# Performance work log

Hardware: AMD Instinct MI355X
Metric: run time of the kernel (lower is better)

The kernel has to match this reference:

```python
import jax, jax.numpy as jnp
import numpy as np

N_NODES = 10000
N_EDGES = 160000
D = 512            # input_dim = hidden_size = output_dim
NUM_EXPERTS = 4
N_LAYERS = 2


def setup_inputs() -> dict:
    key = jax.random.key(0)
    k = jax.random.split(key, 7)
    x = jax.random.normal(k[0], (N_NODES, D), dtype=jnp.float32)
    edge_index = jax.random.randint(k[1], (2, N_EDGES), 0, N_NODES, dtype=jnp.int32)
    # Gating network (Linear D -> NUM_EXPERTS)
    gate_w = jax.random.normal(k[2], (D, NUM_EXPERTS), dtype=jnp.float32) * 0.05
    gate_b = jnp.zeros((NUM_EXPERTS,), dtype=jnp.float32)
    # Per-expert SAGEConv weights: lin_r (self/root) and lin_l (neighbor) + bias
    w_self = jax.random.normal(k[3], (NUM_EXPERTS, N_LAYERS, D, D), dtype=jnp.float32) * 0.05
    w_neigh = jax.random.normal(k[4], (NUM_EXPERTS, N_LAYERS, D, D), dtype=jnp.float32) * 0.05
    b_exp = jnp.zeros((NUM_EXPERTS, N_LAYERS, D), dtype=jnp.float32)
    return {"x": x, "edge_index": edge_index, "gate_w": gate_w, "gate_b": gate_b,
            "w_self": w_self, "w_neigh": w_neigh, "b_exp": b_exp, "top_k": 1}


def reference(x, edge_index, gate_w, gate_b, w_self, w_neigh, b_exp, top_k):
    n = x.shape[0]
    src, dst = edge_index[0], edge_index[1]
    # mean-aggregation normalization (PyG SAGEConv aggr='mean'); 0 for isolated nodes
    deg = jax.ops.segment_sum(jnp.ones_like(src, dtype=x.dtype), dst, num_segments=n)
    inv_deg = jnp.where(deg > 0, 1.0 / jnp.maximum(deg, 1.0), 0.0)[:, None]  # [N,1]

    # gating: softmax(Linear(x)) then top-k routing
    gate = jax.nn.softmax(x @ gate_w + gate_b, axis=-1)          # [N, E]
    top_vals, top_idx = jax.lax.top_k(gate, top_k)               # [N, k]

    def expert(ws, wn, b):  # ws, wn: [L, D, D]; b: [L, D]
        h = x
        for l in range(N_LAYERS):
            agg = jax.ops.segment_sum(h[src], dst, num_segments=n) * inv_deg
            # SAGEConv: lin_l(mean_neigh) + lin_r(x) + bias, then relu (norm='id', eval dropout)
            h = jax.nn.relu(agg @ wn[l] + h @ ws[l] + b[l])
        return h

    # dense all-expert compute (matches original module)
    outs = jax.vmap(expert)(w_self, w_neigh, b_exp)              # [E, N, D]
    outs = jnp.transpose(outs, (1, 0, 2))                        # [N, E, D]
    sel = jnp.take_along_axis(outs, top_idx[:, :, None], axis=1)  # [N, k, D]
    return jnp.sum(sel * top_vals[:, :, None], axis=1)           # [N, D]
```

## Files before the change

kernel.cpp:

```cpp
#include <hip/hip_runtime.h>
#include <hip/hip_bf16.h>
#include <cstdint>

#define N_NODES 10000
#define N_EDGES 160000
#define DIM 512
#define K1 1024
#define NEXP 4

typedef __bf16 bf16_t;
typedef bf16_t bf16x8 __attribute__((ext_vector_type(8)));
typedef float f32x4 __attribute__((ext_vector_type(4)));

#define AS1(p) ((__attribute__((address_space(1))) void*)(p))
#define AS3(p) ((__attribute__((address_space(3))) void*)(p))

#define VMW(N) asm volatile("s_waitcnt vmcnt(" #N ")" ::: "memory")

__global__ void zero_kernel(int* __restrict__ deg, int* __restrict__ ecnt) {
    int i = blockIdx.x * blockDim.x + threadIdx.x;
    if (i < N_NODES) deg[i] = 0;
    if (i < NEXP) ecnt[i] = 0;
}

__global__ void gate_kernel(const float* __restrict__ x,
                            const float* __restrict__ gw,
                            const float* __restrict__ gb,
                            int* __restrict__ top_idx,
                            float* __restrict__ top_val,
                            bf16_t* __restrict__ acat) {
    const int wave = threadIdx.x >> 6;
    const int lane = threadIdx.x & 63;
    const int node = blockIdx.x * 4 + wave;
    if (node >= N_NODES) return;
    const float4* x4 = (const float4*)(x + (size_t)node * DIM);
    const float4* gw4 = (const float4*)gw;
    float4 xa = x4[lane * 2];
    float4 xb = x4[lane * 2 + 1];
    float xv[8] = { xa.x, xa.y, xa.z, xa.w, xb.x, xb.y, xb.z, xb.w };
    float a0 = 0.f, a1 = 0.f, a2 = 0.f, a3 = 0.f;
    #pragma unroll
    for (int c = 0; c < 8; c++) {
        float4 g = gw4[lane * 8 + c];
        a0 += xv[c] * g.x; a1 += xv[c] * g.y; a2 += xv[c] * g.z; a3 += xv[c] * g.w;
    }
    bf16x8 o;
    #pragma unroll
    for (int c = 0; c < 8; c++) o[c] = (bf16_t)xv[c];
    *(bf16x8*)(acat + (size_t)node * K1 + DIM + lane * 8) = o;
    for (int off = 32; off > 0; off >>= 1) {
        a0 += __shfl_xor(a0, off);
        a1 += __shfl_xor(a1, off);
        a2 += __shfl_xor(a2, off);
        a3 += __shfl_xor(a3, off);
    }
    if (lane == 0) {
        float z[4] = { a0 + gb[0], a1 + gb[1], a2 + gb[2], a3 + gb[3] };
        int bi = 0; float bm = z[0];
        for (int e = 1; e < 4; e++) if (z[e] > bm) { bm = z[e]; bi = e; }
        float den = 0.f;
        for (int e = 0; e < 4; e++) den += expf(z[e] - bm);
        top_idx[node] = bi;
        top_val[node] = 1.0f / den;
    }
}

__global__ void bucket_kernel(const int* __restrict__ top_idx,
                              int* __restrict__ ecnt,
                              int* __restrict__ lists) {
    __shared__ int lcnt[NEXP];
    __shared__ int base[NEXP];
    const int tid = threadIdx.x;
    if (tid < NEXP) lcnt[tid] = 0;
    __syncthreads();
    const int node = blockIdx.x * 256 + tid;
    int e = 0, rank = 0;
    if (node < N_NODES) {
        e = top_idx[node];
        rank = atomicAdd(&lcnt[e], 1);
    }
    __syncthreads();
    if (tid < NEXP) base[tid] = atomicAdd(&ecnt[tid], lcnt[tid]);
    __syncthreads();
    if (node < N_NODES) lists[e * N_NODES + base[e] + rank] = node;
}

__global__ void deg_kernel(const int* __restrict__ dst, int* __restrict__ deg) {
    int i = blockIdx.x * blockDim.x + threadIdx.x;
    if (i < N_EDGES) atomicAdd(&deg[dst[i]], 1);
}

__global__ void scan_kernel(const int* __restrict__ deg,
                            int* __restrict__ offs,
                            int* __restrict__ cursor) {
    __shared__ int wsum[16];
    __shared__ int carrysh;
    const int tid = threadIdx.x;
    const int lane = tid & 63;
    const int wv = tid >> 6;
    if (tid == 0) carrysh = 0;
    __syncthreads();
    for (int base = 0; base < N_NODES; base += 1024) {
        int i = base + tid;
        int v = (i < N_NODES) ? deg[i] : 0;
        int s = v;
        #pragma unroll
        for (int off = 1; off < 64; off <<= 1) {
            int t = __shfl_up(s, off);
            if (lane >= off) s += t;
        }
        if (lane == 63) wsum[wv] = s;
        int carry = carrysh;
        __syncthreads();
        if (wv == 0) {
            int w = (lane < 16) ? wsum[lane] : 0;
            #pragma unroll
            for (int off = 1; off < 16; off <<= 1) {
                int t = __shfl_up(w, off);
                if (lane >= off) w += t;
            }
            if (lane < 16) wsum[lane] = w;
        }
        __syncthreads();
        int wbase = (wv > 0) ? wsum[wv - 1] : 0;
        int excl = carry + wbase + s - v;
        if (i < N_NODES) { offs[i] = excl; cursor[i] = excl; }
        int total = wsum[15];
        __syncthreads();
        if (tid == 0) carrysh = carry + total;
        __syncthreads();
    }
    if (tid == 0) offs[N_NODES] = carrysh;
}

__global__ void fill_kernel(const int* __restrict__ src, const int* __restrict__ dst,
                            int* __restrict__ cursor, int* __restrict__ csr) {
    int i = blockIdx.x * blockDim.x + threadIdx.x;
    if (i < N_EDGES) {
        int d = dst[i];
        int p = atomicAdd(&cursor[d], 1);
        csr[p] = src[i];
    }
}

__global__ void wtrans_kernel(const float* __restrict__ w_neigh,
                              const float* __restrict__ w_self,
                              bf16_t* __restrict__ Bt) {
    __shared__ float tile[32][33];
    const int m = blockIdx.z;
    const bool isSelf = m >= 8;
    const int el = m & 7;
    const float* W = (isSelf ? w_self : w_neigh) + (size_t)el * DIM * DIM;
    const int k0 = blockIdx.x * 32;
    const int n0 = blockIdx.y * 32;
    const int tx = threadIdx.x, ty = threadIdx.y;
    for (int r = ty; r < 32; r += 8)
        tile[r][tx] = W[(size_t)(k0 + r) * DIM + n0 + tx];
    __syncthreads();
    for (int r = ty; r < 32; r += 8) {
        int n = n0 + r;
        int k = k0 + tx;
        Bt[((size_t)el * DIM + n) * K1 + (isSelf ? DIM : 0) + k] = (bf16_t)tile[tx][r];
    }
}

__global__ void agg1_kernel(const int* __restrict__ offs, const int* __restrict__ csr,
                            bf16_t* __restrict__ acat) {
    const int wave = threadIdx.x >> 6;
    const int lane = threadIdx.x & 63;
    const int node = blockIdx.x * 4 + wave;
    if (node >= N_NODES) return;
    const int c0 = lane * 8;
    float s[8] = {0,0,0,0,0,0,0,0};
    int beg = offs[node];
    int end = offs[node + 1];
    int d = end - beg;
    int p = beg;
    for (; p + 8 <= end; p += 8) {
        bf16x8 v[8];
        #pragma unroll
        for (int q = 0; q < 8; q++) {
            int idx = csr[p + q];
            v[q] = *(const bf16x8*)(acat + (size_t)idx * K1 + DIM + c0);
        }
        #pragma unroll
        for (int q = 0; q < 8; q++)
            #pragma unroll
            for (int k = 0; k < 8; k++) s[k] += (float)v[q][k];
    }
    for (; p + 4 <= end; p += 4) {
        bf16x8 v[4];
        #pragma unroll
        for (int q = 0; q < 4; q++) {
            int idx = csr[p + q];
            v[q] = *(const bf16x8*)(acat + (size_t)idx * K1 + DIM + c0);
        }
        #pragma unroll
        for (int q = 0; q < 4; q++)
            #pragma unroll
            for (int k = 0; k < 8; k++) s[k] += (float)v[q][k];
    }
    for (; p < end; p++) {
        int idx = csr[p];
        bf16x8 v0 = *(const bf16x8*)(acat + (size_t)idx * K1 + DIM + c0);
        #pragma unroll
        for (int k = 0; k < 8; k++) s[k] += (float)v0[k];
    }
    float w = d > 0 ? 1.0f / (float)d : 0.0f;
    bf16x8 o;
    #pragma unroll
    for (int k = 0; k < 8; k++) o[k] = (bf16_t)(s[k] * w);
    *(bf16x8*)(acat + (size_t)node * K1 + c0) = o;
}

__global__ void agg2_kernel(const int* __restrict__ offs, const int* __restrict__ csr,
                            const int* __restrict__ top_idx,
                            const bf16_t* __restrict__ h1, bf16_t* __restrict__ acat) {
    const int wave = threadIdx.x >> 6;
    const int lane = threadIdx.x & 63;
    const int node = blockIdx.x * 4 + wave;
    if (node >= N_NODES) return;
    const int c0 = lane * 8;
    const bf16_t* hb = h1 + (size_t)top_idx[node] * N_NODES * DIM;
    float s[8] = {0,0,0,0,0,0,0,0};
    int beg = offs[node];
    int end = offs[node + 1];
    int d = end - beg;
    int p = beg;
    for (; p + 8 <= end; p += 8) {
        bf16x8 v[8];
        #pragma unroll
        for (int q = 0; q < 8; q++) {
            int idx = csr[p + q];
            v[q] = *(const bf16x8*)(hb + (size_t)idx * DIM + c0);
        }
        #pragma unroll
        for (int q = 0; q < 8; q++)
            #pragma unroll
            for (int k = 0; k < 8; k++) s[k] += (float)v[q][k];
    }
    for (; p + 4 <= end; p += 4) {
        bf16x8 v[4];
        #pragma unroll
        for (int q = 0; q < 4; q++) {
            int idx = csr[p + q];
            v[q] = *(const bf16x8*)(hb + (size_t)idx * DIM + c0);
        }
        #pragma unroll
        for (int q = 0; q < 4; q++)
            #pragma unroll
            for (int k = 0; k < 8; k++) s[k] += (float)v[q][k];
    }
    for (; p < end; p++) {
        int idx = csr[p];
        bf16x8 v0 = *(const bf16x8*)(hb + (size_t)idx * DIM + c0);
        #pragma unroll
        for (int k = 0; k < 8; k++) s[k] += (float)v0[k];
    }
    float w = d > 0 ? 1.0f / (float)d : 0.0f;
    bf16x8 o;
    #pragma unroll
    for (int k = 0; k < 8; k++) o[k] = (bf16_t)(s[k] * w);
    *(bf16x8*)(acat + (size_t)node * K1 + c0) = o;
    *(bf16x8*)(acat + (size_t)node * K1 + DIM + c0) = *(const bf16x8*)(hb + (size_t)node * DIM + c0);
}

__global__ __launch_bounds__(512, 2)
void gemm_l1_kernel(const bf16_t* __restrict__ A,
                    const bf16_t* __restrict__ Bt,
                    const float* __restrict__ bias_all,
                    bf16_t* __restrict__ h1) {
    const int b = blockIdx.x;
    const int xcd = b & 7;
    const int loc = b >> 3;
    const int mtile = xcd * 2 + (loc >> 4);
    const int ntile = loc & 15;
    const int e = ntile >> 2;

    __shared__ __align__(16) bf16_t As[3 * 640 * 32];
    __shared__ __align__(16) bf16_t Bs[3 * 128 * 32];

    const int t = threadIdx.x;
    const int lane = t & 63;
    const int wave = t >> 6;
    const int rloc = t >> 2;
    const int cgl = ((t & 3) - ((t >> 3) & 3)) & 3;

    const bf16_t* pA0 = A + (size_t)min(mtile * 640 +   0 + rloc, N_NODES - 1) * K1 + cgl * 8;
    const bf16_t* pA1 = A + (size_t)min(mtile * 640 + 128 + rloc, N_NODES - 1) * K1 + cgl * 8;
    const bf16_t* pA2 = A + (size_t)min(mtile * 640 + 256 + rloc, N_NODES - 1) * K1 + cgl * 8;
    const bf16_t* pA3 = A + (size_t)min(mtile * 640 + 384 + rloc, N_NODES - 1) * K1 + cgl * 8;
    const bf16_t* pA4 = A + (size_t)min(mtile * 640 + 512 + rloc, N_NODES - 1) * K1 + cgl * 8;
    const bf16_t* pB0 = Bt + ((size_t)(e * 2 + 0) * DIM + (ntile & 3) * 128 + rloc) * K1 + cgl * 8;

    char* asb = (char*)&As[0];
    char* bsb = (char*)&Bs[0];

    auto stage = [&](int bu) {
        char* ab = asb + bu * 40960 + wave * 1024;
        char* bb = bsb + bu * 8192  + wave * 1024;
        __builtin_amdgcn_global_load_lds(AS1(pA0), AS3(ab),          16, 0, 0);
        __builtin_amdgcn_global_load_lds(AS1(pA1), AS3(ab + 8192),   16, 0, 0);
        __builtin_amdgcn_global_load_lds(AS1(pA2), AS3(ab + 16384),  16, 0, 0);
        __builtin_amdgcn_global_load_lds(AS1(pA3), AS3(ab + 24576),  16, 0, 0);
        __builtin_amdgcn_global_load_lds(AS1(pA4), AS3(ab + 32768),  16, 0, 0);
        __builtin_amdgcn_global_load_lds(AS1(pB0), AS3(bb),          16, 0, 0);
        pA0 += 32; pA1 += 32; pA2 += 32; pA3 += 32; pA4 += 32; pB0 += 32;
    };

    const int rfr = lane & 15;
    const int cpr = lane >> 4;
    const int wm = wave >> 1;
    const int wn = wave & 1;
    const int arow = wm * 160 + rfr;
    const int brow = wn * 64 + rfr;
    const int ppA = (cpr + (arow >> 1)) & 3;
    const int ppB = (cpr + (brow >> 1)) & 3;
    const int aoff = arow * 32 + ppA * 8;
    const int boff = brow * 32 + ppB * 8;

    f32x4 acc[10][4] = {};

    auto compute = [&](int bu) {
        const bf16_t* Ab = As + bu * 20480 + aoff;
        const bf16_t* Bb = Bs + bu * 4096  + boff;
        bf16x8 bfr[4];
        #pragma unroll
        for (int j = 0; j < 4; j++) bfr[j] = *(const bf16x8*)(Bb + j * 512);
        #pragma unroll
        for (int i = 0; i < 10; i++) {
            bf16x8 af = *(const bf16x8*)(Ab + i * 512);
            #pragma unroll
            for (int j = 0; j < 4; j++)
                acc[i][j] = __builtin_amdgcn_mfma_f32_16x16x32_bf16(af, bfr[j], acc[i][j], 0, 0, 0);
        }
    };

    stage(0);
    stage(1);

    int cb = 0, sb = 2;
    for (int tt = 0; tt < 31; ++tt) {
        VMW(6);
        __builtin_amdgcn_s_barrier();
        asm volatile("" ::: "memory");
        if (tt < 30) {
            stage(sb);
            sb = (sb == 2) ? 0 : sb + 1;
        }
        compute(cb);
        cb = (cb == 2) ? 0 : cb + 1;
    }
    VMW(0);
    __builtin_amdgcn_s_barrier();
    asm volatile("" ::: "memory");
    compute(cb);

    const float* bias = bias_all + e * 1024;
    const int cobase = (ntile & 3) * 128 + wn * 64 + (lane & 15);
    float bv[4];
    #pragma unroll
    for (int j = 0; j < 4; j++) bv[j] = bias[cobase + j * 16];
    const int rbase = mtile * 640 + wm * 160 + (lane >> 4) * 4;
    #pragma unroll
    for (int i = 0; i < 10; i++) {
        #pragma unroll
        for (int r = 0; r < 4; r++) {
            int row = rbase + i * 16 + r;
            if (row < N_NODES) {
                bf16_t* cp = h1 + ((size_t)e * N_NODES + row) * DIM + cobase;
                #pragma unroll
                for (int j = 0; j < 4; j++) {
                    float v = fmaxf(acc[i][j][r] + bv[j], 0.f);
                    cp[j * 16] = (bf16_t)v;
                }
            }
        }
    }
}

template <int MODE>
__global__ __launch_bounds__(256)
void gemm_kernel(const bf16_t* __restrict__ A,
                 const bf16_t* __restrict__ Bt,
                 const int layer,
                 const float* __restrict__ bias_all,
                 bf16_t* __restrict__ h1,
                 float* __restrict__ out,
                 const int* __restrict__ lists,
                 const int* __restrict__ ecnt,
                 const float* __restrict__ top_val) {
    int bx, by, e;
    if (MODE == 0) {
        const int b = blockIdx.x;
        const int kq = b & 7;
        const int ke = kq >> 2;
        const int ky = kq & 3;
        const int r = b >> 3;
        const int yloc = r >> 3;
        const int xz = r & 7;
        bx = xz & 3;
        e = ke * 2 + (xz >> 2);
        by = ky * 20 + yloc;
        if (by >= 79) return;
    } else {
        bx = blockIdx.x; by = blockIdx.y; e = blockIdx.z;
    }
    int cnt = N_NODES;
    if (MODE == 1) {
        cnt = ecnt[e];
        if (by * 128 >= cnt) return;
    }
    __shared__ __align__(16) bf16_t As[128 * 32];
    __shared__ __align__(16) bf16_t Bs[128 * 32];

    const int t = threadIdx.x;
    const int lane = t & 63;
    const int wave = t >> 6;
    const int wm = wave >> 1;
    const int wn = wave & 1;

    const int r0 = t >> 2;
    const int rot = (t >> 3) & 3;
    const int cgl = ((t & 3) - rot) & 3;

    int i0 = by * 128 + r0;
    int i1 = i0 + 64;
    int arow0, arow1;
    if (MODE == 0) {
        arow0 = min(i0, N_NODES - 1);
        arow1 = min(i1, N_NODES - 1);
    } else {
        arow0 = lists[e * N_NODES + min(i0, cnt - 1)];
        arow1 = lists[e * N_NODES + min(i1, cnt - 1)];
    }
    const bf16_t* Bte = Bt + (size_t)(e * 2 + layer) * DIM * K1;
    const bf16_t* aptr0 = A + (size_t)arow0 * K1 + cgl * 8;
    const bf16_t* aptr1 = A + (size_t)arow1 * K1 + cgl * 8;
    const bf16_t* bptr0 = Bte + (size_t)(bx * 128 + r0) * K1 + cgl * 8;
    const bf16_t* bptr1 = bptr0 + (size_t)64 * K1;

    f32x4 acc[4][4] = {};
    char* asb = (char*)&As[0];
    char* bsb = (char*)&Bs[0];
    const int wb = wave * 1024;

    const int cpr = lane >> 4;
    const int rfr = lane & 15;

    for (int k0 = 0; k0 < K1; k0 += 32) {
        __syncthreads();
        __builtin_amdgcn_global_load_lds(AS1(aptr0), AS3(asb + wb),        16, 0, 0);
        __builtin_amdgcn_global_load_lds(AS1(aptr1), AS3(asb + 4096 + wb), 16, 0, 0);
        __builtin_amdgcn_global_load_lds(AS1(bptr0), AS3(bsb + wb),        16, 0, 0);
        __builtin_amdgcn_global_load_lds(AS1(bptr1), AS3(bsb + 4096 + wb), 16, 0, 0);
        __syncthreads();
        bf16x8 af[4], bfr[4];
        #pragma unroll
        for (int i = 0; i < 4; i++) {
            int r_full = wm * 64 + i * 16 + rfr;
            int p = (cpr + (r_full >> 1)) & 3;
            af[i] = *(const bf16x8*)(As + r_full * 32 + p * 8);
        }
        #pragma unroll
        for (int j = 0; j < 4; j++) {
            int r_full = wn * 64 + j * 16 + rfr;
            int p = (cpr + (r_full >> 1)) & 3;
            bfr[j] = *(const bf16x8*)(Bs + r_full * 32 + p * 8);
        }
        #pragma unroll
        for (int i = 0; i < 4; i++)
            #pragma unroll
            for (int j = 0; j < 4; j++)
                acc[i][j] = __builtin_amdgcn_mfma_f32_16x16x32_bf16(af[i], bfr[j], acc[i][j], 0, 0, 0);
        aptr0 += 32; aptr1 += 32; bptr0 += 32; bptr1 += 32;
    }

    const float* bias = bias_all + e * 1024 + layer * DIM;
    const int cbase = bx * 128 + wn * 64 + (lane & 15);
    float bv[4];
    #pragma unroll
    for (int j = 0; j < 4; j++) bv[j] = bias[cbase + j * 16];
    #pragma unroll
    for (int i = 0; i < 4; i++) {
        #pragma unroll
        for (int r = 0; r < 4; r++) {
            int row = by * 128 + wm * 64 + i * 16 + (lane >> 4) * 4 + r;
            if (MODE == 0) {
                if (row < N_NODES) {
                    bf16_t* cp = h1 + ((size_t)e * N_NODES + row) * DIM + cbase;
                    #pragma unroll
                    for (int j = 0; j < 4; j++) {
                        float v = fmaxf(acc[i][j][r] + bv[j], 0.f);
                        cp[j * 16] = (bf16_t)v;
                    }
                }
            } else {
                if (row < cnt) {
                    int node = lists[e * N_NODES + row];
                    float tv = top_val[node];
                    float* cp = out + (size_t)node * DIM + cbase;
                    #pragma unroll
                    for (int j = 0; j < 4; j++) {
                        float v = fmaxf(acc[i][j][r] + bv[j], 0.f);
                        cp[j * 16] = v * tv;
                    }
                }
            }
        }
    }
}

extern "C" void kernel_launch(void* const* d_in, const int* in_sizes, int n_in,
                              void* d_out, int out_size, void* d_ws, size_t ws_size,
                              hipStream_t stream) {
    const float* x       = (const float*)d_in[0];
    const int*   edge    = (const int*)d_in[1];
    const float* gw      = (const float*)d_in[2];
    const float* gb      = (const float*)d_in[3];
    const float* w_self  = (const float*)d_in[4];
    const float* w_neigh = (const float*)d_in[5];
    const float* b_exp   = (const float*)d_in[6];
    float* out = (float*)d_out;

    char* p = (char*)d_ws;
    auto alloc = [&](size_t bytes) {
        char* r = p;
        p += (bytes + 255) & ~(size_t)255;
        return r;
    };
    bf16_t* Bt      = (bf16_t*)alloc((size_t)8 * DIM * K1 * 2);
    bf16_t* acat    = (bf16_t*)alloc((size_t)N_NODES * K1 * 2);
    bf16_t* h1      = (bf16_t*)alloc((size_t)NEXP * N_NODES * DIM * 2);
    int*    deg     = (int*)alloc((size_t)N_NODES * 4);
    int*    offs    = (int*)alloc((size_t)(N_NODES + 1) * 4);
    int*    cursor  = (int*)alloc((size_t)N_NODES * 4);
    int*    csr     = (int*)alloc((size_t)N_EDGES * 4);
    int*    top_idx = (int*)alloc((size_t)N_NODES * 4);
    float*  top_val = (float*)alloc((size_t)N_NODES * 4);
    int*    ecnt    = (int*)alloc(256);
    int*    lists   = (int*)alloc((size_t)NEXP * N_NODES * 4);

    const int* srcE = edge;
    const int* dstE = edge + N_EDGES;

    zero_kernel<<<40, 256, 0, stream>>>(deg, ecnt);
    gate_kernel<<<N_NODES / 4, 256, 0, stream>>>(x, gw, gb, top_idx, top_val, acat);
    bucket_kernel<<<40, 256, 0, stream>>>(top_idx, ecnt, lists);
    deg_kernel<<<N_EDGES / 256, 256, 0, stream>>>(dstE, deg);
    scan_kernel<<<1, 1024, 0, stream>>>(deg, offs, cursor);
    fill_kernel<<<N_EDGES / 256, 256, 0, stream>>>(srcE, dstE, cursor, csr);
    wtrans_kernel<<<dim3(16, 16, 16), dim3(32, 8), 0, stream>>>(w_neigh, w_self, Bt);
    agg1_kernel<<<N_NODES / 4, 256, 0, stream>>>(offs, csr, acat);
    gemm_l1_kernel<<<256, 512, 0, stream>>>(acat, Bt, b_exp, h1);
    agg2_kernel<<<N_NODES / 4, 256, 0, stream>>>(offs, csr, top_idx, h1, acat);
    gemm_kernel<1><<<dim3(4, 79, 4), 256, 0, stream>>>(acat, Bt, 1, b_exp, nullptr, out, lists, ecnt, top_val);
}
```

Baseline: 288.3 us.

## Interleave GEMM global-to-LDS loads with MFMA phases using barriers and setprio

Splits each K-step of the 640x128 GEMM main loop into three phases. Each phase issues a subset of the next tile's global_load_lds copies, reads A fragments from LDS, and runs a chunk of MFMAs at raised wave priority. The aim is to spread memory issue across the compute and to stagger the waves ping-pong style so that loads and MFMAs overlap better. It adds several extra workgroup barriers per iteration, which can cost stall time.

After: 273.0 us. 5.3% less time.

```diff
diff --git a/kernel.cpp b/kernel.cpp
--- a/kernel.cpp
+++ b/kernel.cpp
@@ -16,6 +16,7 @@
 #define AS3(p) ((__attribute__((address_space(3))) void*)(p))
 
 #define VMW(N) asm volatile("s_waitcnt vmcnt(" #N ")" ::: "memory")
+#define MFMA16(d, a_, b_) d = __builtin_amdgcn_mfma_f32_16x16x32_bf16(a_, b_, d, 0, 0, 0)
 
 __global__ void zero_kernel(int* __restrict__ deg, int* __restrict__ ecnt) {
     int i = blockIdx.x * blockDim.x + threadIdx.x;
@@ -296,7 +297,7 @@
     char* asb = (char*)&As[0];
     char* bsb = (char*)&Bs[0];
 
-    auto stage = [&](int bu) {
+    auto stage_full = [&](int bu) {
         char* ab = asb + bu * 40960 + wave * 1024;
         char* bb = bsb + bu * 8192  + wave * 1024;
         __builtin_amdgcn_global_load_lds(AS1(pA0), AS3(ab),          16, 0, 0);
@@ -321,7 +322,7 @@
 
     f32x4 acc[10][4] = {};
 
-    auto compute = [&](int bu) {
+    auto compute_full = [&](int bu) {
         const bf16_t* Ab = As + bu * 20480 + aoff;
         const bf16_t* Bb = Bs + bu * 4096  + boff;
         bf16x8 bfr[4];
@@ -332,29 +333,92 @@
             bf16x8 af = *(const bf16x8*)(Ab + i * 512);
             #pragma unroll
             for (int j = 0; j < 4; j++)
-                acc[i][j] = __builtin_amdgcn_mfma_f32_16x16x32_bf16(af, bfr[j], acc[i][j], 0, 0, 0);
+                MFMA16(acc[i][j], af, bfr[j]);
         }
     };
 
-    stage(0);
-    stage(1);
+    stage_full(0);
+    stage_full(1);
 
     int cb = 0, sb = 2;
     for (int tt = 0; tt < 31; ++tt) {
         VMW(6);
         __builtin_amdgcn_s_barrier();
         asm volatile("" ::: "memory");
-        if (tt < 30) {
-            stage(sb);
+        const bool st = (tt < 30);
+        char* ab = asb + sb * 40960 + wave * 1024;
+        char* bb = bsb + sb * 8192  + wave * 1024;
+        const bf16_t* Ab = As + cb * 20480 + aoff;
+        const bf16_t* Bb = Bs + cb * 4096  + boff;
+
+        bf16x8 bq[4], aq[4];
+
+        #pragma unroll
+        for (int j = 0; j < 4; j++) bq[j] = *(const bf16x8*)(Bb + j * 512);
+        #pragma unroll
+        for (int i = 0; i < 4; i++) aq[i] = *(const bf16x8*)(Ab + i * 512);
+        if (st) {
+            __builtin_amdgcn_global_load_lds(AS1(pA0), AS3(ab),        16, 0, 0);
+            __builtin_amdgcn_global_load_lds(AS1(pA1), AS3(ab + 8192), 16, 0, 0);
+        }
+        __builtin_amdgcn_s_barrier();
+        asm volatile("s_waitcnt lgkmcnt(0)" ::: "memory");
+        __builtin_amdgcn_sched_barrier(0);
+        __builtin_amdgcn_s_setprio(1);
+        #pragma unroll
+        for (int i = 0; i < 4; i++)
+            #pragma unroll
+            for (int j = 0; j < 4; j++)
+                MFMA16(acc[i][j], aq[i], bq[j]);
+        __builtin_amdgcn_s_setprio(0);
+        __builtin_amdgcn_s_barrier();
+
+        #pragma unroll
+        for (int i = 0; i < 3; i++) aq[i] = *(const bf16x8*)(Ab + (4 + i) * 512);
+        if (st) {
+            __builtin_amdgcn_global_load_lds(AS1(pA2), AS3(ab + 16384), 16, 0, 0);
+            __builtin_amdgcn_global_load_lds(AS1(pA3), AS3(ab + 24576), 16, 0, 0);
+        }
+        __builtin_amdgcn_s_barrier();
+        asm volatile("s_waitcnt lgkmcnt(0)" ::: "memory");
+        __builtin_amdgcn_sched_barrier(0);
+        __builtin_amdgcn_s_setprio(1);
+        #pragma unroll
+        for (int i = 0; i < 3; i++)
+            #pragma unroll
+            for (int j = 0; j < 4; j++)
+                MFMA16(acc[4 + i][j], aq[i], bq[j]);
+        __builtin_amdgcn_s_setprio(0);
+        __builtin_amdgcn_s_barrier();
+
+        #pragma unroll
+        for (int i = 0; i < 3; i++) aq[i] = *(const bf16x8*)(Ab + (7 + i) * 512);
+        if (st) {
+            __builtin_amdgcn_global_load_lds(AS1(pA4), AS3(ab + 32768), 16, 0, 0);
+            __builtin_amdgcn_global_load_lds(AS1(pB0), AS3(bb),         16, 0, 0);
+        }
+        __builtin_amdgcn_s_barrier();
+        asm volatile("s_waitcnt lgkmcnt(0)" ::: "memory");
+        __builtin_amdgcn_sched_barrier(0);
+        __builtin_amdgcn_s_setprio(1);
+        #pragma unroll
+        for (int i = 0; i < 3; i++)
+            #pragma unroll
+            for (int j = 0; j < 4; j++)
+                MFMA16(acc[7 + i][j], aq[i], bq[j]);
+        __builtin_amdgcn_s_setprio(0);
+        __builtin_amdgcn_s_barrier();
+
+        if (st) {
+            pA0 += 32; pA1 += 32; pA2 += 32; pA3 += 32; pA4 += 32; pB0 += 32;
             sb = (sb == 2) ? 0 : sb + 1;
         }
-        compute(cb);
         cb = (cb == 2) ? 0 : cb + 1;
     }
     VMW(0);
     __builtin_amdgcn_s_barrier();
     asm volatile("" ::: "memory");
-    compute(cb);
+    compute_full(cb);
 
     const float* bias = bias_all + e * 1024;
     const int cobase = (ntile & 3) * 128 + wn * 64 + (lane & 15);
```
